# Performance work log

Measured on AMD Instinct MI355X. Metric: run time of the kernel, lower is better.

## Reference

```python
import jax, jax.numpy as jnp
import numpy as np

H, D = 8, 32            # num_heads, per-head out_dim (same for C1/C2/C3/state)
ALPHA = 0.2             # leaky-relu negative slope
N_C, N_S = 10000, 1024  # nodes per C type, state nodes
E_CC, E_CS = 120000, 10000
IN_C, IN_S = 128, 64


def setup_inputs() -> dict:
    key = jax.random.key(0)
    ks = jax.random.split(key, 20)
    xn = lambda k, sh, s=1.0: jax.random.normal(k, sh, dtype=jnp.float32) * s
    inp = {}
    inp["feat_C1"] = xn(ks[0], (N_C, IN_C))
    inp["feat_C2"] = xn(ks[1], (N_C, IN_C))
    inp["feat_C3"] = xn(ks[2], (N_C, IN_C))
    inp["feat_state"] = xn(ks[3], (N_S, IN_S))
    # linear weights (xavier-ish scale) and zero biases
    inp["W_node"] = xn(ks[4], (3, IN_C, H * D), 0.06)
    inp["b_node"] = jnp.zeros((3, H * D), jnp.float32)
    inp["W_cc"] = xn(ks[5], (9, IN_C, H * D), 0.06)
    inp["b_cc"] = jnp.zeros((9, H * D), jnp.float32)
    inp["W_cs"] = xn(ks[6], (3, IN_C, H * D), 0.06)
    inp["b_cs"] = jnp.zeros((3, H * D), jnp.float32)
    inp["W_in"] = xn(ks[7], (IN_S, H * D), 0.08)
    inp["b_in"] = jnp.zeros((H * D,), jnp.float32)
    # attention vectors: [..., 0] = src vec, [..., 1] = dst vec
    inp["attn_cc"] = xn(ks[8], (9, 2, H, D), 0.3)
    inp["attn_cs"] = xn(ks[9], (3, 2, H, D), 0.3)
    # edge lists; relation r = 3*src_type + dst_type for cc
    inp["edges_cc_src"] = jax.random.randint(ks[10], (9, E_CC), 0, N_C, dtype=jnp.int32)
    inp["edges_cc_dst"] = jax.random.randint(ks[11], (9, E_CC), 0, N_C, dtype=jnp.int32)
    inp["edges_cs_src"] = jax.random.randint(ks[12], (3, E_CS), 0, N_C, dtype=jnp.int32)
    inp["edges_cs_dst"] = jax.random.randint(ks[13], (3, E_CS), 0, N_S, dtype=jnp.int32)
    return inp


def _segment_softmax(e, dst, n):
    # e: [E, H]; softmax over edges sharing the same dst node (DGL edge_softmax)
    m = jax.ops.segment_max(e, dst, num_segments=n)
    ex = jnp.exp(e - m[dst])
    s = jax.ops.segment_sum(ex, dst, num_segments=n)
    return ex / s[dst]


def _gat_relation(Wh_src, Wh_dst_self, a_src_vec, a_dst_vec, src, dst, n_dst):
    # Wh_src: [Ns,H,D] projected src feats for this relation
    # Wh_dst_self: [Nd,H,D] dst-type self projection (used for dst attention)
    a_s = jnp.sum(Wh_src * a_src_vec, axis=-1)       # [Ns,H]
    a_d = jnp.sum(Wh_dst_self * a_dst_vec, axis=-1)  # [Nd,H]
    e = jax.nn.leaky_relu(a_s[src] + a_d[dst], ALPHA)   # [E,H]
    a = _segment_softmax(e, dst, n_dst)                 # [E,H]
    msg = Wh_src[src] * a[:, :, None]                   # [E,H,D]
    return jax.ops.segment_sum(msg, dst, num_segments=n_dst)


def _forward(feat_C1, feat_C2, feat_C3, feat_state, W_node, b_node, W_cc, b_cc,
             W_cs, b_cs, W_in, b_in, attn_cc, attn_cs,
             edges_cc_src, edges_cc_dst, edges_cs_src, edges_cs_dst):
    feats_c = [feat_C1, feat_C2, feat_C3]
    n_c = [f.shape[0] for f in feats_c]
    # self projections (used as dst attention features)
    Wh_node = [(feats_c[t] @ W_node[t] + b_node[t]).reshape(-1, H, D) for t in range(3)]
    out_c = [jnp.zeros_like(Wh_node[t]) for t in range(3)]
    # 9 C->C relations: r = 3*s + d
    for r in range(9):
        s, d = divmod(r, 3)
        Wh = (feats_c[s] @ W_cc[r] + b_cc[r]).reshape(-1, H, D)
        ft = _gat_relation(Wh, Wh_node[d], attn_cc[r, 0], attn_cc[r, 1],
                           edges_cc_src[r], edges_cc_dst[r], n_c[d])
        out_c[d] = out_c[d] + ft
    # state: 'in' self projection + 3 C->state relations
    Wh_in = (feat_state @ W_in + b_in).reshape(-1, H, D)
    out_s = Wh_in
    n_s = feat_state.shape[0]
    for t in range(3):
        Wh = (feats_c[t] @ W_cs[t] + b_cs[t]).reshape(-1, H, D)
        ft = _gat_relation(Wh, Wh_in, attn_cs[t, 0], attn_cs[t, 1],
                           edges_cs_src[t], edges_cs_dst[t], n_s)
        out_s = out_s + ft
    relu = jax.nn.relu
    return (relu(out_c[0]), relu(out_c[1]), relu(out_c[2]), relu(out_s))


def reference(feat_C1, feat_C2, feat_C3, feat_state, W_node, b_node, W_cc, b_cc,
              W_cs, b_cs, W_in, b_in, attn_cc, attn_cs,
              edges_cc_src, edges_cc_dst, edges_cs_src, edges_cs_dst):
    return _forward(feat_C1, feat_C2, feat_C3, feat_state, W_node, b_node, W_cc,
                    b_cc, W_cs, b_cs, W_in, b_in, attn_cc, attn_cs,
                    edges_cc_src, edges_cc_dst, edges_cs_src, edges_cs_dst)
```

## Files before the change

### kernel.cpp

```cpp
#include <hip/hip_runtime.h>


#define H_ 8
#define D_ 32
#define HD 256
#define NC 10000
#define NS 1024
#define INC 128
#define INS 64
#define ECC 120000
#define ECS 10000
#define ALPHA 0.2f
#define CAP 64

typedef unsigned short u16;
typedef __attribute__((ext_vector_type(8))) short short8;
typedef __attribute__((ext_vector_type(4))) float f32x4;
typedef __attribute__((ext_vector_type(2))) float f32x2;

static constexpr size_t WHB_CC = 0;
static constexpr size_t WHB_CS = 23040000;
static constexpr size_t WHB_IN = 30720000;
static constexpr size_t FB0  = 15491072;
static constexpr size_t ASCC = FB0;
static constexpr size_t ADCC = FB0 + 720000;
static constexpr size_t ASCS = FB0 + 1440000;
static constexpr size_t ADCS = FB0 + 1680000;
static constexpr size_t BAF  = FB0 + 1704576;
static constexpr size_t FBC  = 34437760;
static constexpr size_t FBS  = 38277760;
static constexpr size_t WTCC = 38343296;
static constexpr size_t WTCS = 38638208;
static constexpr size_t WTIN = 38736512;
static constexpr size_t WAT  = 38752896;
static constexpr size_t IBYTE = 77768704;
static constexpr size_t SBYTE = 78140992;

static constexpr int TOTE  = 9 * ECC + 3 * ECS;
static constexpr int NB_Z0 = 91;
static constexpr int NB_FT = 3814;
static constexpr int NB_WT = 104;
static constexpr int NB_FO = 32;
static constexpr int NB_K2 = 2710;

__device__ __forceinline__ u16 f2b(float f) {
  unsigned u = __float_as_uint(f);
  return (u16)((u + 0x7FFFu + ((u >> 16) & 1u)) >> 16);
}
__device__ __forceinline__ float bl(unsigned u) { return __uint_as_float(u << 16); }
__device__ __forceinline__ float bh(unsigned u) { return __uint_as_float(u & 0xffff0000u); }

__global__ __launch_bounds__(256) void k_prep(
    const float* f1, const float* f2, const float* f3, const float* fs,
    const float* Wcc, const float* Wcs, const float* Win, const float* Wnode,
    const float* bcc, const float* bnode, const float* bcs, const float* bin,
    const float* accv, const float* acsv,
    u16* wsu, float* wsf, int* cnts) {
  __shared__ float Ls[64 * 65];
  int b = blockIdx.x, t = threadIdx.x;
  if (b < NB_Z0) {
    int i = b * 256 + t;
    if (i < 23268) ((int4*)cnts)[i] = make_int4(0, 0, 0, 0);
    return;
  }
  b -= NB_Z0;
  if (b < NB_FT) {
    const float* src; u16* dst; int idx, n4;
    if (b < 3750) {
      int ty = b / 1250;
      src = (ty == 0) ? f1 : (ty == 1) ? f2 : f3;
      dst = wsu + FBC + (size_t)ty * 1280000;
      idx = (b - ty * 1250) * 256 + t; n4 = 320000;
    } else {
      src = fs; dst = wsu + FBS; idx = (b - 3750) * 256 + t; n4 = 16384;
    }
    if (idx < n4) {
      float4 v = ((const float4*)src)[idx];
      uint2 o;
      o.x = (unsigned)f2b(v.x) | ((unsigned)f2b(v.y) << 16);
      o.y = (unsigned)f2b(v.z) | ((unsigned)f2b(v.w) << 16);
      *(uint2*)(dst + (size_t)idx * 4) = o;
    }
    return;
  }
  b -= NB_FT;
  if (b < NB_WT) {
    int mat = b >> 3, sub = b & 7;
    int K = (mat == 12) ? INS : INC;
    if (mat == 12 && sub >= 4) return;
    int k0 = (sub >> 2) * 64, n0 = (sub & 3) * 64;
    const float* src; u16* dst;
    if (mat < 9)        { src = Wcc + (size_t)mat * INC * HD;        dst = wsu + WTCC + (size_t)mat * 32768; }
    else if (mat < 12)  { src = Wcs + (size_t)(mat - 9) * INC * HD;  dst = wsu + WTCS + (size_t)(mat - 9) * 32768; }
    else                { src = Win;                                 dst = wsu + WTIN; }
    #pragma unroll
    for (int it = 0; it < 4; it++) {
      int idx = t + it * 256;
      int r = idx >> 4, c4 = idx & 15;
      float4 v = *(const float4*)&src[(size_t)(k0 + r) * HD + n0 + c4 * 4];
      Ls[r * 65 + c4 * 4 + 0] = v.x; Ls[r * 65 + c4 * 4 + 1] = v.y;
      Ls[r * 65 + c4 * 4 + 2] = v.z; Ls[r * 65 + c4 * 4 + 3] = v.w;
    }
    __syncthreads();
    int n = t >> 2, k8 = (t & 3) * 16;
    unsigned o[8];
    #pragma unroll
    for (int j = 0; j < 8; j++) {
      u16 lo = f2b(Ls[(k8 + 2 * j) * 65 + n]);
      u16 hi = f2b(Ls[(k8 + 2 * j + 1) * 65 + n]);
      o[j] = (unsigned)lo | ((unsigned)hi << 16);
    }
    uint4* dp = (uint4*)&dst[(size_t)(n0 + n) * K + k0 + k8];
    dp[0] = make_uint4(o[0], o[1], o[2], o[3]);
    dp[1] = make_uint4(o[4], o[5], o[6], o[7]);
    return;
  }
  b -= NB_WT;
  int tile = b >> 3, sub = b & 7;
  int K = (tile == 3) ? INS : INC;
  int c0 = sub * 8;
  for (int idx = t; idx < 8 * K; idx += 256) {
    int col = c0 + idx / K, k = idx % K;
    int m = col >> 3, h = col & 7;
    const float* W = nullptr; const float* av = nullptr;
    if (tile < 3) {
      if (m < 3)      { int r = 3*tile + m; W = Wcc + (size_t)r*INC*HD;   av = accv + (size_t)r*512 + h*32; }
      else if (m < 6) { int r = 3*(m-3) + tile; W = Wnode + (size_t)tile*INC*HD; av = accv + (size_t)r*512 + 256 + h*32; }
      else if (m == 6){ W = Wcs + (size_t)tile*INC*HD; av = acsv + (size_t)tile*512 + h*32; }
    } else if (m < 3) { W = Win; av = acsv + (size_t)m*512 + 256 + h*32; }
    float s = 0.f;
    if (W) {
      const float* wp = W + (size_t)k * HD + h * 32;
      #pragma unroll 8
      for (int d = 0; d < 32; d++) s += wp[d] * av[d];
    }
    wsu[WAT + (size_t)tile * 8192 + (size_t)col * K + k] = f2b(s);
  }
  if (sub == 0 && t < 64) {
    int col = t, m = col >> 3, h = col & 7;
    const float* bb = nullptr; const float* av = nullptr;
    if (tile < 3) {
      if (m < 3)      { int r = 3*tile + m; bb = bcc + (size_t)r*HD;  av = accv + (size_t)r*512 + h*32; }
      else if (m < 6) { int r = 3*(m-3) + tile; bb = bnode + (size_t)tile*HD; av = accv + (size_t)r*512 + 256 + h*32; }
      else if (m == 6){ bb = bcs + (size_t)tile*HD; av = acsv + (size_t)tile*512 + h*32; }
    } else if (m < 3) { bb = bin; av = acsv + (size_t)m*512 + 256 + h*32; }
    float s = 0.f;
    if (bb) for (int d = 0; d < 32; d++) s += bb[h*32 + d] * av[d];
    wsf[BAF + tile * 64 + col] = s;
  }
}

__global__ __launch_bounds__(256, 2) void k_fuse(
    u16* wsu, float* wsf, const float* bcc, const float* bcs, const float* bin,
    const int* eccs, const int* eccd, const int* ecss, const int* ecsd,
    int* cnts, u16* slt) {
  __shared__ __align__(16) char smem[69632];
  int gb = blockIdx.x, t = threadIdx.x;
  if ((gb % 5) == 4) {
    int k = gb / 5;
    int i0 = (k * 256 + t) * 8;
    if (i0 >= TOTE) return;
    int dd[8], ss[8], p[8];
    int cbase;
    if (i0 < 9 * ECC) {
      int r = i0 / ECC;
      int4 d0 = *(const int4*)&eccd[i0]; int4 d1 = *(const int4*)&eccd[i0 + 4];
      int4 s0 = *(const int4*)&eccs[i0]; int4 s1 = *(const int4*)&eccs[i0 + 4];
      dd[0]=d0.x; dd[1]=d0.y; dd[2]=d0.z; dd[3]=d0.w;
      dd[4]=d1.x; dd[5]=d1.y; dd[6]=d1.z; dd[7]=d1.w;
      ss[0]=s0.x; ss[1]=s0.y; ss[2]=s0.z; ss[3]=s0.w;
      ss[4]=s1.x; ss[5]=s1.y; ss[6]=s1.z; ss[7]=s1.w;
      cbase = r * NC;
    } else {
      int u0 = i0 - 9 * ECC;
      int r = u0 / ECS;
      int4 d0 = *(const int4*)&ecsd[u0]; int4 d1 = *(const int4*)&ecsd[u0 + 4];
      int4 s0 = *(const int4*)&ecss[u0]; int4 s1 = *(const int4*)&ecss[u0 + 4];
      dd[0]=d0.x; dd[1]=d0.y; dd[2]=d0.z; dd[3]=d0.w;
      dd[4]=d1.x; dd[5]=d1.y; dd[6]=d1.z; dd[7]=d1.w;
      ss[0]=s0.x; ss[1]=s0.y; ss[2]=s0.z; ss[3]=s0.w;
      ss[4]=s1.x; ss[5]=s1.y; ss[6]=s1.z; ss[7]=s1.w;
      cbase = 90000 + r * NS;
    }
    #pragma unroll
    for (int q = 0; q < 8; q++) p[q] = atomicAdd(&cnts[cbase + dd[q]], 1);
    #pragma unroll
    for (int q = 0; q < 8; q++)
      if (p[q] < CAP) slt[((size_t)(cbase + dd[q])) * CAP + p[q]] = (u16)ss[q];
    return;
  }
  int g = 4 * (gb / 5) + (gb % 5);
  if (g >= 2157) return;
  u16* As = (u16*)smem;
  u16* Bs = (u16*)(smem + 34816);
  const u16 *A, *Bt; const float* bias = nullptr; u16* C = nullptr;
  int M, K, r0, n0 = 0, ty = 0;
  bool isScore = false;
  if (g < 1896) {
    int z = g / 158, rem = g - z * 158;
    int by = rem / 79, bx = rem - by * 79;
    r0 = bx * 128; n0 = by * 128; M = NC; K = 128;
    if (z < 9) { A = wsu + FBC + (size_t)(z/3)*1280000; Bt = wsu + WTCC + (size_t)z*32768; bias = bcc + (size_t)z*HD; C = wsu + WHB_CC + (size_t)z*NC*HD; }
    else { int q = z - 9; A = wsu + FBC + (size_t)q*1280000; Bt = wsu + WTCS + (size_t)q*32768; bias = bcs + (size_t)q*HD; C = wsu + WHB_CS + (size_t)q*NC*HD; }
  } else if (g < 1912) {
    int loc = g - 1896; int by = loc / 8, bx = loc - by * 8;
    r0 = bx * 128; n0 = by * 128; M = NS; K = 64;
    A = wsu + FBS; Bt = wsu + WTIN; bias = bin; C = wsu + WHB_IN;
  } else if (g < 2149) {
    isScore = true; ty = (g - 1912) / 79; int bx = (g - 1912) % 79;
    r0 = bx * 128; M = NC; K = 128;
    A = wsu + FBC + (size_t)ty * 1280000; Bt = wsu + WAT + (size_t)ty * 8192;
  } else {
    isScore = true; ty = 3; int bx = g - 2149;
    r0 = bx * 128; M = NS; K = 64;
    A = wsu + FBS; Bt = wsu + WAT + (size_t)3 * 8192;
  }
  int SA = K + 8;
  int NB = isScore ? 64 : 128;
  {
    int ksh = (K == 128) ? 4 : 3;
    int kmask = (1 << ksh) - 1;
    int sc8 = SA >> 3;
    const uint4* ga = (const uint4*)(A + (size_t)r0 * K);
    const uint4* gb2 = (const uint4*)(Bt + (size_t)n0 * K);
    uint4* la = (uint4*)As; uint4* lb = (uint4*)Bs;
    int tota = (128 * K) >> 3, totb = (NB * K) >> 3;
    for (int i = t; i < tota; i += 256) la[(i >> ksh) * sc8 + (i & kmask)] = ga[i];
    for (int i = t; i < totb; i += 256) lb[(i >> ksh) * sc8 + (i & kmask)] = gb2[i];
  }
  __syncthreads();
  int lane = t & 63, w = t >> 6, l16 = lane & 15, quad = lane >> 4;
  int arow0 = w * 32 + l16;
  if (!isScore) {
    f32x4 acc[2][8];
    #pragma unroll
    for (int i = 0; i < 2; i++)
      #pragma unroll
      for (int j = 0; j < 8; j++) acc[i][j] = (f32x4){0.f, 0.f, 0.f, 0.f};
    for (int ks = 0; ks < K; ks += 32) {
      int ko = ks + quad * 8;
      short8 a0 = *(const short8*)&As[(size_t)arow0 * SA + ko];
      short8 a1 = *(const short8*)&As[(size_t)(arow0 + 16) * SA + ko];
      #pragma unroll
      for (int j = 0; j < 8; j++) {
        short8 bfr = *(const short8*)&Bs[(size_t)(j * 16 + l16) * SA + ko];
        acc[0][j] = __builtin_amdgcn_mfma_f32_16x16x32_bf16(a0, bfr, acc[0][j], 0, 0, 0);
        acc[1][j] = __builtin_amdgcn_mfma_f32_16x16x32_bf16(a1, bfr, acc[1][j], 0, 0, 0);
      }
    }
    __syncthreads();
    float* Cl = (float*)smem;
    #pragma unroll
    for (int i = 0; i < 2; i++) {
      int rl0 = w * 32 + i * 16 + quad * 4;
      #pragma unroll
      for (int j = 0; j < 8; j++) {
        int cl = j * 16 + l16;
        float bv = bias[n0 + cl];
        #pragma unroll
        for (int rg = 0; rg < 4; rg++)
          Cl[(rl0 + rg) * 132 + cl] = acc[i][j][rg] + bv;
      }
    }
    __syncthreads();
    for (int task = t; task < 2048; task += 256) {
      int row = task >> 4, seg = task & 15;
      int gr = r0 + row;
      if (gr >= M) continue;
      const float* cp = Cl + row * 132 + seg * 8;
      float4 v0 = *(const float4*)cp;
      float4 v1 = *(const float4*)(cp + 4);
      uint4 o;
      o.x = (unsigned)f2b(v0.x) | ((unsigned)f2b(v0.y) << 16);
      o.y = (unsigned)f2b(v0.z) | ((unsigned)f2b(v0.w) << 16);
      o.z = (unsigned)f2b(v1.x) | ((unsigned)f2b(v1.y) << 16);
      o.w = (unsigned)f2b(v1.z) | ((unsigned)f2b(v1.w) << 16);
      *(uint4*)&C[(size_t)gr * HD + n0 + seg * 8] = o;
    }
  } else {
    f32x4 acc[2][4];
    #pragma unroll
    for (int i = 0; i < 2; i++)
      #pragma unroll
      for (int j = 0; j < 4; j++) acc[i][j] = (f32x4){0.f, 0.f, 0.f, 0.f};
    for (int ks = 0; ks < K; ks += 32) {
      int ko = ks + quad * 8;
      short8 a0 = *(const short8*)&As[(size_t)arow0 * SA + ko];
      short8 a1 = *(const short8*)&As[(size_t)(arow0 + 16) * SA + ko];
      #pragma unroll
      for (int j = 0; j < 4; j++) {
        short8 bfr = *(const short8*)&Bs[(size_t)(j * 16 + l16) * SA + ko];
        acc[0][j] = __builtin_amdgcn_mfma_f32_16x16x32_bf16(a0, bfr, acc[0][j], 0, 0, 0);
        acc[1][j] = __builtin_amdgcn_mfma_f32_16x16x32_bf16(a1, bfr, acc[1][j], 0, 0, 0);
      }
    }
    float* sp[4]; float bav[4];
    #pragma unroll
    for (int j = 0; j < 4; j++) {
      int col = j * 16 + l16;
      int m = col >> 3, h = col & 7;
      float* p = nullptr;
      if (ty < 3) {
        if (m < 3)       p = wsf + ASCC + (size_t)(3*ty + m) * NC * H_;
        else if (m < 6)  p = wsf + ADCC + (size_t)(3*(m-3) + ty) * NC * H_;
        else if (m == 6) p = wsf + ASCS + (size_t)ty * NC * H_;
      } else if (m < 3)  p = wsf + ADCS + (size_t)m * NS * H_;
      sp[j] = p ? (p + h) : nullptr;
      bav[j] = wsf[BAF + ty * 64 + col];
    }
    #pragma unroll
    for (int i = 0; i < 2; i++) {
      int rl0 = w * 32 + i * 16 + quad * 4;
      #pragma unroll
      for (int j = 0; j < 4; j++) {
        if (!sp[j]) continue;
        #pragma unroll
        for (int rg = 0; rg < 4; rg++) {
          int gr = r0 + rl0 + rg;
          if (gr < M) sp[j][(size_t)gr * 8] = (acc[i][j][rg] + bav[j]) * 1.44269504089f;
        }
      }
    }
  }
}

__global__ __launch_bounds__(256) void k_agg(const u16* wsu, const float* wsf,
                                             const int* cnts, const u16* slt,
                                             float* out) {
  int t = threadIdx.x, lane = t & 63, w = t >> 6;
  int node = blockIdx.x * 4 + w;
  int l3 = lane >> 3;
  int h7 = lane & 7;
  int lb = lane * 8;
  f32x2 totA = {0.f, 0.f}, totB = {0.f, 0.f};
  bool isC = node < 3 * NC;
  int dtype = 0, n;
  if (isC) { dtype = node / NC; n = node - dtype * NC; } else { n = node - 3 * NC; }
  for (int j = 0; j < 3; j++) {
    int cidx; const float* ASp; const float* ADp; const char* wb;
    if (isC) {
      int r = j * 3 + dtype;
      cidx = r * NC + n;
      ASp = wsf + ASCC + (size_t)r * NC * H_;
      ADp = wsf + ADCC + (size_t)r * NC * H_;
      wb  = (const char*)(wsu + WHB_CC + (size_t)r * NC * HD);
    } else {
      cidx = 90000 + j * NS + n;
      ASp = wsf + ASCS + (size_t)j * NC * H_;
      ADp = wsf + ADCS + (size_t)j * NS * H_;
      wb  = (const char*)(wsu + WHB_CS + (size_t)j * NC * HD);
    }
    int cnt = min(cnts[cidx], CAP);
    if (cnt <= 0) continue;
    int srcid = (int)slt[(size_t)cidx * CAP + min(lane, cnt - 1)];
    float adn = ADp[(size_t)n * H_ + h7];
    f32x2 aA = {0.f, 0.f}, aB = {0.f, 0.f};
    float zac = 0.f;
    float wcur;
    {
      int ce = min(l3, cnt - 1);
      int sid = __shfl(srcid, ce);
      float sc = ASp[(size_t)sid * H_ + h7] + adn;
      sc = fmaxf(sc, ALPHA * sc);
      wcur = (l3 < cnt) ? __builtin_amdgcn_exp2f(sc) : 0.f;
    }
    for (int g = 0; g < cnt; g += 8) {
      uint2 mreg[8];
      #pragma unroll
      for (int ee = 0; ee < 8; ee++) {
        int ce = min(g + ee, cnt - 1);
        int sre = __builtin_amdgcn_readlane(srcid, ce);
        mreg[ee] = *(const uint2*)(wb + ((size_t)sre << 9) + lb);
      }
      float wold = wcur;
      zac += wold;
      if (g + 8 < cnt) {
        int e = g + 8 + l3;
        int ce = min(e, cnt - 1);
        int sid = __shfl(srcid, ce);
        float sc = ASp[(size_t)sid * H_ + h7] + adn;
        sc = fmaxf(sc, ALPHA * sc);
        wcur = (e < cnt) ? __builtin_amdgcn_exp2f(sc) : 0.f;
      }
      #pragma unroll
      for (int ee = 0; ee < 8; ee++) {
        float we = __shfl(wold, ee * 8 + l3);
        f32x2 q0, q1;
        q0.x = bl(mreg[ee].x); q0.y = bh(mreg[ee].x);
        q1.x = bl(mreg[ee].y); q1.y = bh(mreg[ee].y);
        aA += q0 * we;
        aB += q1 * we;
      }
    }
    zac += __shfl_xor(zac, 8);
    zac += __shfl_xor(zac, 16);
    zac += __shfl_xor(zac, 32);
    float inv = 1.f / zac;
    float invp = __shfl(inv, l3);
    totA += aA * invp;
    totB += aB * invp;
  }
  if (!isC) {
    uint2 m = *(const uint2*)((const char*)(wsu + WHB_IN) + (size_t)n * 512 + lb);
    totA.x += bl(m.x); totA.y += bh(m.x);
    totB.x += bl(m.y); totB.y += bh(m.y);
  }
  float4 v = make_float4(fmaxf(totA.x, 0.f), fmaxf(totA.y, 0.f),
                         fmaxf(totB.x, 0.f), fmaxf(totB.y, 0.f));
  *(float4*)(out + (size_t)node * HD + lane * 4) = v;
}

extern "C" void kernel_launch(void* const* d_in, const int* in_sizes, int n_in,
                              void* d_out, int out_size, void* d_ws, size_t ws_size,
                              hipStream_t stream) {
  (void)in_sizes; (void)n_in; (void)out_size; (void)ws_size;
  const float* f1    = (const float*)d_in[0];
  const float* f2    = (const float*)d_in[1];
  const float* f3    = (const float*)d_in[2];
  const float* fs    = (const float*)d_in[3];
  const float* Wnode = (const float*)d_in[4];
  const float* bnode = (const float*)d_in[5];
  const float* Wcc   = (const float*)d_in[6];
  const float* bcc   = (const float*)d_in[7];
  const float* Wcs   = (const float*)d_in[8];
  const float* bcs   = (const float*)d_in[9];
  const float* Win   = (const float*)d_in[10];
  const float* bin   = (const float*)d_in[11];
  const float* accv  = (const float*)d_in[12];
  const float* acsv  = (const float*)d_in[13];
  const int* eccs    = (const int*)d_in[14];
  const int* eccd    = (const int*)d_in[15];
  const int* ecss    = (const int*)d_in[16];
  const int* ecsd    = (const int*)d_in[17];
  float* wsf = (float*)d_ws;
  u16*   wsu = (u16*)d_ws;
  int*   cnts = (int*)((char*)d_ws + IBYTE);
  u16*   slt  = (u16*)((char*)d_ws + SBYTE);
  float* out = (float*)d_out;

  k_prep<<<dim3(NB_Z0 + NB_FT + NB_WT + NB_FO), 256, 0, stream>>>(
      f1, f2, f3, fs, Wcc, Wcs, Win, Wnode, bcc, bnode, bcs, bin, accv, acsv,
      wsu, wsf, cnts);
  k_fuse<<<dim3(NB_K2), 256, 0, stream>>>(
      wsu, wsf, bcc, bcs, bin, eccs, eccd, ecss, ecsd, cnts, slt);
  k_agg<<<dim3((3 * NC + NS) / 4), 256, 0, stream>>>(wsu, wsf, cnts, slt, out);
}
```

Before: 254.2 us.

## Precompute attention weights into LDS and double-buffer gathers across relations

The aggregation kernel now computes all softmax weights for the three relations up front and stores them in per-wave shared memory, so they are read from LDS rather than broadcast with shuffles. Gathers of source rows are double-buffered, and the first group of the next relation is prefetched while the current one is consumed, so load latency overlaps the FMAs. In exchange it adds 24KB of LDS per block and more live registers for the two buffers, which may lower occupancy.

```diff
diff --git a/kernel.cpp b/kernel.cpp
--- a/kernel.cpp
+++ b/kernel.cpp
@@ -324,89 +324,122 @@
   }
 }
 
+__device__ __forceinline__ void loadg8(uint2* buf, int srcv, int cl, int g,
+                                       const char* wb, int lb) {
+  #pragma unroll
+  for (int ee = 0; ee < 8; ee++) {
+    int sre = __builtin_amdgcn_readlane(srcv, min(g + ee, cl));
+    buf[ee] = *(const uint2*)(wb + ((size_t)(unsigned)sre << 9) + lb);
+  }
+}
+__device__ __forceinline__ void consume8(const uint2* buf, const float* wp,
+                                         f32x2& sA, f32x2& sB) {
+  #pragma unroll
+  for (int ee = 0; ee < 8; ee++) {
+    float wv = wp[ee * 8];
+    f32x2 q0, q1;
+    q0.x = bl(buf[ee].x); q0.y = bh(buf[ee].x);
+    q1.x = bl(buf[ee].y); q1.y = bh(buf[ee].y);
+    sA += q0 * wv;
+    sB += q1 * wv;
+  }
+}
+
 __global__ __launch_bounds__(256) void k_agg(const u16* wsu, const float* wsf,
                                              const int* cnts, const u16* slt,
                                              float* out) {
+  __shared__ float Wsm[4 * 1536];
   int t = threadIdx.x, lane = t & 63, w = t >> 6;
   int node = blockIdx.x * 4 + w;
-  int l3 = lane >> 3;
-  int h7 = lane & 7;
+  int l3 = lane >> 3, h7 = lane & 7;
   int lb = lane * 8;
-  f32x2 totA = {0.f, 0.f}, totB = {0.f, 0.f};
+  float* Wv = Wsm + w * 1536;
   bool isC = node < 3 * NC;
   int dtype = 0, n;
   if (isC) { dtype = node / NC; n = node - dtype * NC; } else { n = node - 3 * NC; }
+
+  int cidx[3]; const float* ASp[3]; const float* adnp[3]; const char* wb[3];
+  #pragma unroll
   for (int j = 0; j < 3; j++) {
-    int cidx; const float* ASp; const float* ADp; const char* wb;
     if (isC) {
       int r = j * 3 + dtype;
-      cidx = r * NC + n;
-      ASp = wsf + ASCC + (size_t)r * NC * H_;
-      ADp = wsf + ADCC + (size_t)r * NC * H_;
-      wb  = (const char*)(wsu + WHB_CC + (size_t)r * NC * HD);
+      cidx[j] = r * NC + n;
+      ASp[j]  = wsf + ASCC + (size_t)r * NC * H_;
+      adnp[j] = wsf + ADCC + (size_t)r * NC * H_ + (size_t)n * H_ + h7;
+      wb[j]   = (const char*)(wsu + WHB_CC + (size_t)r * NC * HD);
     } else {
-      cidx = 90000 + j * NS + n;
-      ASp = wsf + ASCS + (size_t)j * NC * H_;
-      ADp = wsf + ADCS + (size_t)j * NS * H_;
-      wb  = (const char*)(wsu + WHB_CS + (size_t)j * NC * HD);
-    }
-    int cnt = min(cnts[cidx], CAP);
-    if (cnt <= 0) continue;
-    int srcid = (int)slt[(size_t)cidx * CAP + min(lane, cnt - 1)];
-    float adn = ADp[(size_t)n * H_ + h7];
-    f32x2 aA = {0.f, 0.f}, aB = {0.f, 0.f};
+      cidx[j] = 90000 + j * NS + n;
+      ASp[j]  = wsf + ASCS + (size_t)j * NC * H_;
+      adnp[j] = wsf + ADCS + (size_t)j * NS * H_ + (size_t)n * H_ + h7;
+      wb[j]   = (const char*)(wsu + WHB_CS + (size_t)j * NC * HD);
+    }
+  }
+  int cnt[3], clm[3], srcv[3]; float adn[3];
+  #pragma unroll
+  for (int j = 0; j < 3; j++) cnt[j] = min(cnts[cidx[j]], CAP);
+  #pragma unroll
+  for (int j = 0; j < 3; j++) {
+    clm[j] = max(cnt[j] - 1, 0);
+    srcv[j] = (int)slt[(size_t)cidx[j] * CAP + min(lane, clm[j])];
+  }
+  #pragma unroll
+  for (int j = 0; j < 3; j++) adn[j] = *adnp[j];
+
+  uint2 cur[8], nxt[8];
+  loadg8(cur, srcv[0], clm[0], 0, wb[0], lb);
+
+  float invp[3];
+  #pragma unroll
+  for (int j = 0; j < 3; j++) {
     float zac = 0.f;
-    float wcur;
-    {
-      int ce = min(l3, cnt - 1);
-      int sid = __shfl(srcid, ce);
-      float sc = ASp[(size_t)sid * H_ + h7] + adn;
+    int c = cnt[j];
+    for (int g = 0; g < c; g += 8) {
+      int e = g + l3;
+      int sid = __shfl(srcv[j], min(e, clm[j]));
+      float sc = ASp[j][(size_t)sid * H_ + h7] + adn[j];
       sc = fmaxf(sc, ALPHA * sc);
-      wcur = (l3 < cnt) ? __builtin_amdgcn_exp2f(sc) : 0.f;
-    }
-    for (int g = 0; g < cnt; g += 8) {
-      uint2 mreg[8];
-      #pragma unroll
-      for (int ee = 0; ee < 8; ee++) {
-        int ce = min(g + ee, cnt - 1);
-        int sre = __builtin_amdgcn_readlane(srcid, ce);
-        mreg[ee] = *(const uint2*)(wb + ((size_t)sre << 9) + lb);
-      }
-      float wold = wcur;
-      zac += wold;
-      if (g + 8 < cnt) {
-        int e = g + 8 + l3;
-        int ce = min(e, cnt - 1);
-        int sid = __shfl(srcid, ce);
-        float sc = ASp[(size_t)sid * H_ + h7] + adn;
-        sc = fmaxf(sc, ALPHA * sc);
-        wcur = (e < cnt) ? __builtin_amdgcn_exp2f(sc) : 0.f;
-      }
-      #pragma unroll
-      for (int ee = 0; ee < 8; ee++) {
-        float we = __shfl(wold, ee * 8 + l3);
-        f32x2 q0, q1;
-        q0.x = bl(mreg[ee].x); q0.y = bh(mreg[ee].x);
-        q1.x = bl(mreg[ee].y); q1.y = bh(mreg[ee].y);
-        aA += q0 * we;
-        aB += q1 * we;
-      }
+      float wv = (e < c) ? __builtin_amdgcn_exp2f(sc) : 0.f;
+      zac += wv;
+      Wv[j * 512 + g * 8 + lane] = wv;
     }
     zac += __shfl_xor(zac, 8);
     zac += __shfl_xor(zac, 16);
     zac += __shfl_xor(zac, 32);
     float inv = 1.f / zac;
-    float invp = __shfl(inv, l3);
-    totA += aA * invp;
-    totB += aB * invp;
-  }
+    invp[j] = (c > 0) ? __shfl(inv, l3) : 0.f;
+  }
+
+  f32x2 tA = {0.f, 0.f}, tB = {0.f, 0.f};
+#define RELBODY(J, JN, LAST)                                                 \
+  {                                                                          \
+    int c = cnt[J];                                                          \
+    if (c > 0) {                                                             \
+      f32x2 sA = {0.f, 0.f}, sB = {0.f, 0.f};                                \
+      for (int g = 0; g < c; g += 8) {                                       \
+        if (g + 8 < c) loadg8(nxt, srcv[J], clm[J], g + 8, wb[J], lb);       \
+        else if (!(LAST)) loadg8(nxt, srcv[JN], clm[JN], 0, wb[JN], lb);     \
+        consume8(cur, Wv + (J) * 512 + g * 8 + l3, sA, sB);                  \
+        _Pragma("unroll")                                                    \
+        for (int ee = 0; ee < 8; ee++) cur[ee] = nxt[ee];                    \
+      }                                                                      \
+      tA += sA * invp[J];                                                    \
+      tB += sB * invp[J];                                                    \
+    } else if (!(LAST)) {                                                    \
+      loadg8(cur, srcv[JN], clm[JN], 0, wb[JN], lb);                         \
+    }                                                                        \
+  }
+  RELBODY(0, 1, false)
+  RELBODY(1, 2, false)
+  RELBODY(2, 2, true)
+#undef RELBODY
+
   if (!isC) {
     uint2 m = *(const uint2*)((const char*)(wsu + WHB_IN) + (size_t)n * 512 + lb);
-    totA.x += bl(m.x); totA.y += bh(m.x);
-    totB.x += bl(m.y); totB.y += bh(m.y);
-  }
-  float4 v = make_float4(fmaxf(totA.x, 0.f), fmaxf(totA.y, 0.f),
-                         fmaxf(totB.x, 0.f), fmaxf(totB.y, 0.f));
+    tA.x += bl(m.x); tA.y += bh(m.x);
+    tB.x += bl(m.y); tB.y += bh(m.y);
+  }
+  float4 v = make_float4(fmaxf(tA.x, 0.f), fmaxf(tA.y, 0.f),
+                         fmaxf(tB.x, 0.f), fmaxf(tB.y, 0.f));
   *(float4*)(out + (size_t)node * HD + lane * 4) = v;
 }
 
```

Result: slower. 265.5 us (+4.4%).
